# Performance work log

Measured on AMD Instinct MI355X. Metric: run time of the kernel, lower is better.

The kernel has to match this reference:

```python
import jax, jax.numpy as jnp
import numpy as np

N_NODES = 50000
N_EDGES = 600000
NODE_DIM = 128
HID = 128
NUM_LAYERS = 3


def setup_inputs() -> dict:
    key = jax.random.key(0)
    ks = jax.random.split(key, 16)
    s = lambda fan_in: 1.0 / np.sqrt(fan_in)
    inp = {
        'node_features': jax.random.normal(ks[0], (N_NODES, NODE_DIM), dtype=jnp.float32),
        'edge_index': jax.random.randint(ks[1], (2, N_EDGES), 0, N_NODES, dtype=jnp.int64 if jax.config.jax_enable_x64 else jnp.int32),
        # node embedding
        'W_emb': jax.random.uniform(ks[2], (NODE_DIM, HID), jnp.float32, -s(NODE_DIM), s(NODE_DIM)),
        'b_emb': jnp.zeros((HID,), jnp.float32),
        # gnn layers (stacked over layer axis)
        'W_gnn': jax.random.uniform(ks[3], (NUM_LAYERS, HID, HID), jnp.float32, -s(HID), s(HID)),
        'b_gnn': jnp.zeros((NUM_LAYERS, HID), jnp.float32),
        # edge mask generator
        'W_m1': jax.random.uniform(ks[4], (2 * HID, HID), jnp.float32, -s(2 * HID), s(2 * HID)),
        'b_m1': jnp.zeros((HID,), jnp.float32),
        'W_m2': jax.random.uniform(ks[5], (HID, 1), jnp.float32, -s(HID), s(HID)),
        'b_m2': jnp.zeros((1,), jnp.float32),
        # predictor
        'W_p1': jax.random.uniform(ks[6], (HID, HID), jnp.float32, -s(HID), s(HID)),
        'b_p1': jnp.zeros((HID,), jnp.float32),
        'W_p2': jax.random.uniform(ks[7], (HID, 1), jnp.float32, -s(HID), s(HID)),
        'b_p2': jnp.zeros((1,), jnp.float32),
    }
    return inp


def _edge_mask(h, src, dst, W_m1, b_m1, W_m2, b_m2):
    # per-edge gather + concat -> 2-layer MLP -> sigmoid importance
    ef = jnp.concatenate([h[src], h[dst]], axis=1)          # [E, 2H]
    imp = jax.nn.sigmoid(jax.nn.relu(ef @ W_m1 + b_m1) @ W_m2 + b_m2)[:, 0]  # [E]
    # eval mode: temp=2.0, offset=0.4
    return jax.nn.sigmoid((imp - 0.4) * 2.0)


def reference(node_features, edge_index, W_emb, b_emb, W_gnn, b_gnn,
              W_m1, b_m1, W_m2, b_m2, W_p1, b_p1, W_p2, b_p2):
    src, dst = edge_index[0], edge_index[1]
    n = node_features.shape[0]
    h = jax.nn.relu(node_features @ W_emb + b_emb)           # [N, H]
    mask = _edge_mask(h, src, dst, W_m1, b_m1, W_m2, b_m2)    # [E]
    for i in range(NUM_LAYERS):
        msgs = jax.ops.segment_sum(h[src] * mask[:, None], dst, num_segments=n)  # scatter-add
        h = jax.nn.relu((h + msgs) @ W_gnn[i] + b_gnn[i])
        if i < NUM_LAYERS - 1:
            mask = _edge_mask(h, src, dst, W_m1, b_m1, W_m2, b_m2)
    prediction = jax.nn.relu(h[0] @ W_p1 + b_p1) @ W_p2 + b_p2  # [1]
    return prediction, mask, h
```

## Files before the change

### kernel.cpp

```cpp
#include <hip/hip_runtime.h>
#include <hip/hip_bf16.h>

#define NN 50000
#define NE 600000
#define HD 128
#define DET_SAMPLES 65536
#define NBLK 196
#define GGRID4 ((NN + 15)/16)
#define LDT 136

typedef unsigned short ushort_t;
typedef __attribute__((ext_vector_type(8))) short short8v;
typedef __attribute__((ext_vector_type(4))) float f32x4;

__device__ __forceinline__ float sigmoidf_(float x){ return 1.f/(1.f+__expf(-x)); }

__device__ __forceinline__ ushort_t f2bf(float f){
  unsigned int u = __float_as_uint(f);
  unsigned int r = (u + 0x7FFFu + ((u >> 16) & 1u)) >> 16;
  return (ushort_t)r;
}

__device__ __forceinline__ float bflo(unsigned u){ return __uint_as_float(u << 16); }
__device__ __forceinline__ float bfhi(unsigned u){ return __uint_as_float(u & 0xFFFF0000u); }

__global__ void write_scalar_kernel(float* __restrict__ p, float v){ p[0] = v; }

__global__ void detect_kernel(const unsigned int* __restrict__ w, int* __restrict__ flag){
  int i = blockIdx.x*256 + threadIdx.x;
  int z = (w[2*i + 1] == 0u) ? 1 : 0;
  atomicAdd(flag, z);
}

__global__ void extract_kernel(const void* __restrict__ ei, const int* __restrict__ flag,
                               int* __restrict__ srcW, int* __restrict__ dstW,
                               int* __restrict__ counts){
  const int e = blockIdx.x*256 + threadIdx.x;
  if (e >= NE) return;
  int s, d;
  if (*flag > (DET_SAMPLES/2)){
    const long long* p = (const long long*)ei;
    s = (int)p[e]; d = (int)p[NE + e];
  } else {
    const int* p = (const int*)ei;
    s = p[e]; d = p[NE + e];
  }
  srcW[e] = s; dstW[e] = d;
  atomicAdd(&counts[d], 1);
}

__global__ __launch_bounds__(256) void scanA_kernel(const int* __restrict__ counts,
                                                    int* __restrict__ partial){
  __shared__ int s[256];
  const int t = threadIdx.x;
  const int idx = blockIdx.x*256 + t;
  s[t] = (idx < NN) ? counts[idx] : 0;
  __syncthreads();
  for (int off = 128; off > 0; off >>= 1){
    if (t < off) s[t] += s[t + off];
    __syncthreads();
  }
  if (t == 0) partial[blockIdx.x] = s[0];
}

__global__ __launch_bounds__(256) void scanB_kernel(const int* __restrict__ partial,
                                                    int* __restrict__ bOff){
  __shared__ int s[256];
  const int t = threadIdx.x;
  const int v = (t < NBLK) ? partial[t] : 0;
  s[t] = v;
  __syncthreads();
  for (int off = 1; off < 256; off <<= 1){
    int add = (t >= off) ? s[t - off] : 0;
    __syncthreads();
    s[t] += add;
    __syncthreads();
  }
  if (t < NBLK) bOff[t] = s[t] - v;
}

__global__ __launch_bounds__(256) void scanC_kernel(const int* __restrict__ counts,
    const int* __restrict__ bOff, int* __restrict__ row_start, int* __restrict__ cursor){
  __shared__ int s[256];
  const int t = threadIdx.x;
  const int idx = blockIdx.x*256 + t;
  const int c = (idx < NN) ? counts[idx] : 0;
  s[t] = c;
  __syncthreads();
  for (int off = 1; off < 256; off <<= 1){
    int add = (t >= off) ? s[t - off] : 0;
    __syncthreads();
    s[t] += add;
    __syncthreads();
  }
  const int excl = bOff[blockIdx.x] + s[t] - c;
  if (idx < NN){ row_start[idx] = excl; cursor[idx] = excl; }
  else if (idx == NN){ row_start[NN] = excl; }
}

__global__ void fill_kernel(const int* __restrict__ dstI, const int* __restrict__ srcI,
                            int* __restrict__ cursor, int* __restrict__ eids,
                            int* __restrict__ srcS){
  int e = blockIdx.x*256 + threadIdx.x;
  if (e < NE){
    int p = atomicAdd(&cursor[dstI[e]], 1);
    eids[p] = e;
    srcS[p] = srcI[e];
  }
}

__global__ __launch_bounds__(256) void wcvt_all_kernel(const float* __restrict__ Wemb,
    const float* __restrict__ Wgnn, const float* __restrict__ Wm1,
    ushort_t* __restrict__ WtAll){
  const int idx = blockIdx.x*256 + threadIdx.x;
  const int m = idx >> 14;
  const int r = idx & 16383;
  const int k = r >> 7, n = r & 127;
  const float* W = (m == 0) ? Wemb : (m <= 3) ? (Wgnn + (size_t)(m-1)*16384)
                                              : (Wm1  + (size_t)(m-4)*16384);
  WtAll[(size_t)m*16384 + n*HD + k] = f2bf(W[r]);
}

template<int F32A>
__global__ __launch_bounds__(256) void gemm_fused(const void* __restrict__ inP,
    const ushort_t* __restrict__ Wt, const float* __restrict__ bias,
    float* __restrict__ outF, ushort_t* __restrict__ outB,
    const ushort_t* __restrict__ WtU, const ushort_t* __restrict__ WtV,
    const float* __restrict__ biasU, ushort_t* __restrict__ outU,
    ushort_t* __restrict__ outV, int n, int doRelu)
{
  __shared__ ushort_t hT[16*LDT];
  const int cq   = threadIdx.x >> 6;
  const int lane = threadIdx.x & 63;
  const int fr = lane & 15;
  const int fq = lane >> 4;
  const int row0 = blockIdx.x*16;
  const int arow = row0 + fr;
  const bool rowok = (arow < n);
  f32x4 acc[2];
  acc[0] = (f32x4)0.0f; acc[1] = (f32x4)0.0f;
  #pragma unroll
  for (int ks = 0; ks < 4; ++ks){
    const int k0 = ks*32 + fq*8;
    short8v af = (short8v)0;
    if (rowok){
      if (F32A){
        const float* in = (const float*)inP;
        const float4 a0 = *(const float4*)(in + (size_t)arow*HD + k0);
        const float4 a1 = *(const float4*)(in + (size_t)arow*HD + k0 + 4);
        af[0]=(short)f2bf(a0.x); af[1]=(short)f2bf(a0.y);
        af[2]=(short)f2bf(a0.z); af[3]=(short)f2bf(a0.w);
        af[4]=(short)f2bf(a1.x); af[5]=(short)f2bf(a1.y);
        af[6]=(short)f2bf(a1.z); af[7]=(short)f2bf(a1.w);
      } else {
        const ushort_t* inB = (const ushort_t*)inP;
        af = *(const short8v*)(inB + (size_t)arow*HD + k0);
      }
    }
    #pragma unroll
    for (int tcl = 0; tcl < 2; ++tcl){
      const int tc = cq*2 + tcl;
      const short8v bf = *(const short8v*)(Wt + (size_t)(tc*16 + fr)*HD + k0);
      acc[tcl] = __builtin_amdgcn_mfma_f32_16x16x32_bf16(af, bf, acc[tcl], 0, 0, 0);
    }
  }
  #pragma unroll
  for (int tcl = 0; tcl < 2; ++tcl){
    const int col = (cq*2 + tcl)*16 + fr;
    const float b = bias ? bias[col] : 0.f;
    #pragma unroll
    for (int j = 0; j < 4; ++j){
      const int r = row0 + fq*4 + j;
      float x = acc[tcl][j] + b;
      if (doRelu) x = fmaxf(x, 0.f);
      const ushort_t xb = (r < n) ? f2bf(x) : (ushort_t)0;
      if (WtU) hT[(fq*4 + j)*LDT + col] = xb;
      if (r < n){
        if (outF) outF[(size_t)r*HD + col] = x;
        if (outB) outB[(size_t)r*HD + col] = xb;
      }
    }
  }
  if (WtU){
    __syncthreads();
    f32x4 aU[2], aV[2];
    aU[0] = (f32x4)0.0f; aU[1] = (f32x4)0.0f;
    aV[0] = (f32x4)0.0f; aV[1] = (f32x4)0.0f;
    #pragma unroll
    for (int ks = 0; ks < 4; ++ks){
      const int k0 = ks*32 + fq*8;
      const short8v af = *(const short8v*)(hT + fr*LDT + k0);
      #pragma unroll
      for (int tcl = 0; tcl < 2; ++tcl){
        const int tc = cq*2 + tcl;
        const short8v bu = *(const short8v*)(WtU + (size_t)(tc*16 + fr)*HD + k0);
        aU[tcl] = __builtin_amdgcn_mfma_f32_16x16x32_bf16(af, bu, aU[tcl], 0, 0, 0);
        const short8v bv = *(const short8v*)(WtV + (size_t)(tc*16 + fr)*HD + k0);
        aV[tcl] = __builtin_amdgcn_mfma_f32_16x16x32_bf16(af, bv, aV[tcl], 0, 0, 0);
      }
    }
    #pragma unroll
    for (int tcl = 0; tcl < 2; ++tcl){
      const int col = (cq*2 + tcl)*16 + fr;
      const float b = biasU[col];
      #pragma unroll
      for (int j = 0; j < 4; ++j){
        const int r = row0 + fq*4 + j;
        if (r >= n) continue;
        outU[(size_t)r*HD + col] = f2bf(aU[tcl][j] + b);
        outV[(size_t)r*HD + col] = f2bf(aV[tcl][j]);
      }
    }
  }
}

__global__ __launch_bounds__(256) void mask_msg_kernel(
    const ushort_t* __restrict__ U, const ushort_t* __restrict__ V,
    const ushort_t* __restrict__ hB,
    ushort_t* __restrict__ hB2,
    const int* __restrict__ srcS, const int* __restrict__ eidS,
    const int* __restrict__ row_start,
    const float* __restrict__ Wm2, const float* __restrict__ bm2,
    float* __restrict__ maskOut)
{
  const int v = blockIdx.x*4 + (threadIdx.x >> 6);
  const int lane = threadIdx.x & 63;
  const int g   = lane >> 4;
  const int sub = lane & 15;
  const float4 wA = ((const float4*)Wm2)[sub*2];
  const float4 wB = ((const float4*)Wm2)[sub*2+1];
  const float b2 = bm2[0];
  const uint4 vv = ((const uint4*)(V + (size_t)v*HD))[sub];
  float a0=0.f,a1=0.f,a2=0.f,a3=0.f,a4=0.f,a5=0.f,a6=0.f,a7=0.f;
  const int beg = row_start[v], end = row_start[v+1];
  int idx = beg + g;
  uint4 uu = make_uint4(0,0,0,0), hh = make_uint4(0,0,0,0);
  int e0 = 0;
  if (idx < end){
    const int s = srcS[idx];
    if (maskOut) e0 = eidS[idx];
    uu = ((const uint4*)(U  + (size_t)s*HD))[sub];
    hh = ((const uint4*)(hB + (size_t)s*HD))[sub];
  }
  while (idx < end){
    const int nidx = idx + 4;
    uint4 uuN = make_uint4(0,0,0,0), hhN = make_uint4(0,0,0,0);
    int eN = 0;
    if (nidx < end){
      const int sn = srcS[nidx];
      if (maskOut) eN = eidS[nidx];
      uuN = ((const uint4*)(U  + (size_t)sn*HD))[sub];
      hhN = ((const uint4*)(hB + (size_t)sn*HD))[sub];
    }
    float p;
    p = fmaxf(bflo(uu.x)+bflo(vv.x), 0.f) * wA.x;
    p = fmaf(fmaxf(bfhi(uu.x)+bfhi(vv.x), 0.f), wA.y, p);
    p = fmaf(fmaxf(bflo(uu.y)+bflo(vv.y), 0.f), wA.z, p);
    p = fmaf(fmaxf(bfhi(uu.y)+bfhi(vv.y), 0.f), wA.w, p);
    p = fmaf(fmaxf(bflo(uu.z)+bflo(vv.z), 0.f), wB.x, p);
    p = fmaf(fmaxf(bfhi(uu.z)+bfhi(vv.z), 0.f), wB.y, p);
    p = fmaf(fmaxf(bflo(uu.w)+bflo(vv.w), 0.f), wB.z, p);
    p = fmaf(fmaxf(bfhi(uu.w)+bfhi(vv.w), 0.f), wB.w, p);
    p += __shfl_xor(p, 1, 64);
    p += __shfl_xor(p, 2, 64);
    p += __shfl_xor(p, 4, 64);
    p += __shfl_xor(p, 8, 64);
    const float imp = sigmoidf_(p + b2);
    const float mk  = sigmoidf_((imp - 0.4f) * 2.0f);
    if (maskOut != nullptr && sub == 0) maskOut[e0] = mk;
    a0 = fmaf(mk, bflo(hh.x), a0);
    a1 = fmaf(mk, bfhi(hh.x), a1);
    a2 = fmaf(mk, bflo(hh.y), a2);
    a3 = fmaf(mk, bfhi(hh.y), a3);
    a4 = fmaf(mk, bflo(hh.z), a4);
    a5 = fmaf(mk, bfhi(hh.z), a5);
    a6 = fmaf(mk, bflo(hh.w), a6);
    a7 = fmaf(mk, bfhi(hh.w), a7);
    uu = uuN; hh = hhN; e0 = eN; idx = nidx;
  }
  a0 += __shfl_xor(a0, 16, 64); a0 += __shfl_xor(a0, 32, 64);
  a1 += __shfl_xor(a1, 16, 64); a1 += __shfl_xor(a1, 32, 64);
  a2 += __shfl_xor(a2, 16, 64); a2 += __shfl_xor(a2, 32, 64);
  a3 += __shfl_xor(a3, 16, 64); a3 += __shfl_xor(a3, 32, 64);
  a4 += __shfl_xor(a4, 16, 64); a4 += __shfl_xor(a4, 32, 64);
  a5 += __shfl_xor(a5, 16, 64); a5 += __shfl_xor(a5, 32, 64);
  a6 += __shfl_xor(a6, 16, 64); a6 += __shfl_xor(a6, 32, 64);
  a7 += __shfl_xor(a7, 16, 64); a7 += __shfl_xor(a7, 32, 64);
  if (g == 0){
    const uint4 hrow = ((const uint4*)(hB + (size_t)v*HD))[sub];
    const float x0 = bflo(hrow.x) + a0, x1 = bfhi(hrow.x) + a1;
    const float x2 = bflo(hrow.y) + a2, x3 = bfhi(hrow.y) + a3;
    const float x4 = bflo(hrow.z) + a4, x5 = bfhi(hrow.z) + a5;
    const float x6 = bflo(hrow.w) + a6, x7 = bfhi(hrow.w) + a7;
    ushort4 p0, p1;
    p0.x = f2bf(x0); p0.y = f2bf(x1); p0.z = f2bf(x2); p0.w = f2bf(x3);
    p1.x = f2bf(x4); p1.y = f2bf(x5); p1.z = f2bf(x6); p1.w = f2bf(x7);
    ushort4* hb2row = (ushort4*)(hB2 + (size_t)v*HD) + sub*2;
    hb2row[0] = p0;
    hb2row[1] = p1;
  }
}

__global__ __launch_bounds__(128) void pred_kernel(const float* __restrict__ h,
  const float* __restrict__ Wp1, const float* __restrict__ bp1,
  const float* __restrict__ Wp2, const float* __restrict__ bp2,
  float* __restrict__ out0)
{
  __shared__ float red[128];
  const int t = threadIdx.x;
  float s = bp1[t];
  for (int k = 0; k < HD; ++k) s = fmaf(h[k], Wp1[k*HD + t], s);
  s = fmaxf(s, 0.f) * Wp2[t];
  red[t] = s;
  __syncthreads();
  for (int off = 64; off > 0; off >>= 1){
    if (t < off) red[t] += red[t + off];
    __syncthreads();
  }
  if (t == 0) out0[0] = red[0] + bp2[0];
}

extern "C" void kernel_launch(void* const* d_in, const int* in_sizes, int n_in,
                              void* d_out, int out_size, void* d_ws, size_t ws_size,
                              hipStream_t stream)
{
  (void)out_size;
  float* fOut = (float*)d_out;
  float* predOut = fOut;
  float* maskOut = fOut + 1;
  float* hOut    = fOut + 1 + NE;

  static const int expSizes[14] = {6400000,1200000,16384,128,49152,384,32768,128,128,1,
                                   16384,128,128,1};
  const size_t NEEDED = 87100000;
  float diag = 0.f;
  if (n_in != 14) diag = 900.f + (float)n_in;
  else {
    for (int i = 0; i < 14; ++i)
      if (in_sizes[i] != expSizes[i]){ diag = 200.f + 16.f*(float)i; break; }
  }
  if (diag == 0.f && ws_size < NEEDED) diag = 5000.f + (float)(ws_size >> 20);

  if (diag != 0.f){
    write_scalar_kernel<<<1, 1, 0, stream>>>(predOut, diag);
    return;
  }

  const float* nf   = (const float*)d_in[0];
  const void*  ei   = d_in[1];
  const float* Wemb = (const float*)d_in[2];
  const float* bemb = (const float*)d_in[3];
  const float* Wgnn = (const float*)d_in[4];
  const float* bgnn = (const float*)d_in[5];
  const float* Wm1  = (const float*)d_in[6];
  const float* bm1  = (const float*)d_in[7];
  const float* Wm2  = (const float*)d_in[8];
  const float* bm2  = (const float*)d_in[9];
  const float* Wp1  = (const float*)d_in[10];
  const float* bp1  = (const float*)d_in[11];
  const float* Wp2  = (const float*)d_in[12];
  const float* bp2  = (const float*)d_in[13];

  float* hA    = (float*)d_ws;
  float* tmpU  = hA   + (size_t)NN*HD;
  float* Vbuf  = tmpU + (size_t)NN*HD;
  float* srcSf = Vbuf + (size_t)NN*HD;
  int* srcS    = (int*)srcSf;
  int* row_start = srcS + NE;
  int* cursor  = row_start + (NN + 1);
  int* counts  = cursor + NN;
  int* eids    = counts + NN;
  int* srcW    = eids + NE;
  int* dstW    = srcW + NE;
  int* flag    = dstW + NE;
  int* partial = flag + 1;
  int* bOff    = partial + NBLK;

  ushort_t* Ub  = (ushort_t*)tmpU;
  ushort_t* hB2 = (ushort_t*)tmpU + (size_t)NN*HD;
  ushort_t* Vb  = (ushort_t*)Vbuf;
  ushort_t* hB  = (ushort_t*)Vbuf + (size_t)NN*HD;

  ushort_t* WtAll = (ushort_t*)cursor;
  ushort_t* WtEmb = WtAll;
  ushort_t* WtG0  = WtAll + 1*16384;
  ushort_t* WtG1  = WtAll + 2*16384;
  ushort_t* WtG2  = WtAll + 3*16384;
  ushort_t* WtU   = WtAll + 4*16384;
  ushort_t* WtV   = WtAll + 5*16384;

  hipMemsetAsync(flag, 0, sizeof(int), stream);
  hipMemsetAsync(counts, 0, NN*sizeof(int), stream);
  detect_kernel<<<DET_SAMPLES/256, 256, 0, stream>>>((const unsigned int*)ei, flag);
  extract_kernel<<<(NE + 255)/256, 256, 0, stream>>>(ei, flag, srcW, dstW, counts);

  scanA_kernel<<<NBLK, 256, 0, stream>>>(counts, partial);
  scanB_kernel<<<1, 256, 0, stream>>>(partial, bOff);
  scanC_kernel<<<NBLK, 256, 0, stream>>>(counts, bOff, row_start, cursor);
  fill_kernel<<<(NE + 255)/256, 256, 0, stream>>>(dstW, srcW, cursor, eids, srcS);

  wcvt_all_kernel<<<384, 256, 0, stream>>>(Wemb, Wgnn, Wm1, WtAll);

  gemm_fused<1><<<GGRID4, 256, 0, stream>>>(nf, WtEmb, bemb, nullptr, hB,
                                            WtU, WtV, bm1, Ub, Vb, NN, 1);

  const ushort_t* WtG[3] = {WtG0, WtG1, WtG2};
  for (int L = 0; L < 3; ++L){
    float* mOut = (L < 2) ? nullptr : maskOut;
    mask_msg_kernel<<<NN/4, 256, 0, stream>>>(Ub, Vb, hB, hB2, srcS, eids, row_start,
                                              Wm2, bm2, mOut);
    if (L < 2){
      gemm_fused<0><<<GGRID4, 256, 0, stream>>>(hB2, WtG[L], bgnn + (size_t)L*HD,
                                                nullptr, hB, WtU, WtV, bm1, Ub, Vb,
                                                NN, 1);
    } else {
      gemm_fused<0><<<GGRID4, 256, 0, stream>>>(hB2, WtG[2], bgnn + 2*HD,
                                                hOut, nullptr, nullptr, nullptr,
                                                nullptr, nullptr, nullptr, NN, 1);
    }
  }

  pred_kernel<<<1, 128, 0, stream>>>(hOut, Wp1, bp1, Wp2, bp2, predOut);
}
```

Measured before the change: 437.2 us.

## Make GEMM blocks persistent and keep weight fragments in registers across tiles

The fused node GEMM now launches a fixed grid of 782 blocks. Each block loops over up to four 16-row tiles, and the W, Wu and Wv fragments plus biases are loaded into registers once per block instead of once per tile. Bounds checks are dropped because N is a multiple of 16, and the last layer gets a dedicated gemm_final kernel. This removes repeated weight loads from L2 in exchange for higher register pressure (launch_bounds 256,3) and fewer resident blocks.

```diff
diff --git a/kernel.cpp b/kernel.cpp
--- a/kernel.cpp
+++ b/kernel.cpp
@@ -6,7 +6,8 @@
 #define HD 128
 #define DET_SAMPLES 65536
 #define NBLK 196
-#define GGRID4 ((NN + 15)/16)
+#define NTILES 3125
+#define GPERS 782
 #define LDT 136
 
 typedef unsigned short ushort_t;
@@ -121,29 +122,53 @@
   WtAll[(size_t)m*16384 + n*HD + k] = f2bf(W[r]);
 }
 
-template<int F32A>
-__global__ __launch_bounds__(256) void gemm_fused(const void* __restrict__ inP,
+template<int F32A, int DOUV>
+__global__ __launch_bounds__(256, 3) void gemm_fused(const void* __restrict__ inP,
     const ushort_t* __restrict__ Wt, const float* __restrict__ bias,
     float* __restrict__ outF, ushort_t* __restrict__ outB,
     const ushort_t* __restrict__ WtU, const ushort_t* __restrict__ WtV,
     const float* __restrict__ biasU, ushort_t* __restrict__ outU,
-    ushort_t* __restrict__ outV, int n, int doRelu)
+    ushort_t* __restrict__ outV)
 {
   __shared__ ushort_t hT[16*LDT];
   const int cq   = threadIdx.x >> 6;
   const int lane = threadIdx.x & 63;
   const int fr = lane & 15;
   const int fq = lane >> 4;
-  const int row0 = blockIdx.x*16;
-  const int arow = row0 + fr;
-  const bool rowok = (arow < n);
-  f32x4 acc[2];
-  acc[0] = (f32x4)0.0f; acc[1] = (f32x4)0.0f;
+  short8v bh[4][2];
   #pragma unroll
-  for (int ks = 0; ks < 4; ++ks){
-    const int k0 = ks*32 + fq*8;
-    short8v af = (short8v)0;
-    if (rowok){
+  for (int ks = 0; ks < 4; ++ks)
+    #pragma unroll
+    for (int tcl = 0; tcl < 2; ++tcl)
+      bh[ks][tcl] = *(const short8v*)(Wt + (size_t)((cq*2+tcl)*16 + fr)*HD + ks*32 + fq*8);
+  short8v bu[4][2], bv[4][2];
+  if (DOUV){
+    #pragma unroll
+    for (int ks = 0; ks < 4; ++ks)
+      #pragma unroll
+      for (int tcl = 0; tcl < 2; ++tcl){
+        bu[ks][tcl] = *(const short8v*)(WtU + (size_t)((cq*2+tcl)*16 + fr)*HD + ks*32 + fq*8);
+        bv[ks][tcl] = *(const short8v*)(WtV + (size_t)((cq*2+tcl)*16 + fr)*HD + ks*32 + fq*8);
+      }
+  }
+  float bb[2], bub[2];
+  #pragma unroll
+  for (int tcl = 0; tcl < 2; ++tcl){
+    const int col = (cq*2 + tcl)*16 + fr;
+    bb[tcl]  = bias ? bias[col] : 0.f;
+    bub[tcl] = DOUV ? biasU[col] : 0.f;
+  }
+
+  for (int it = 0; it < 4; ++it){
+    const int tile = blockIdx.x + it*GPERS;
+    if (tile >= NTILES) break;
+    const int row0 = tile*16;
+    const int arow = row0 + fr;
+    f32x4 acc0 = (f32x4)0.0f, acc1 = (f32x4)0.0f;
+    #pragma unroll
+    for (int ks = 0; ks < 4; ++ks){
+      const int k0 = ks*32 + fq*8;
+      short8v af;
       if (F32A){
         const float* in = (const float*)inP;
         const float4 a0 = *(const float4*)(in + (size_t)arow*HD + k0);
@@ -156,60 +181,49 @@
         const ushort_t* inB = (const ushort_t*)inP;
         af = *(const short8v*)(inB + (size_t)arow*HD + k0);
       }
+      acc0 = __builtin_amdgcn_mfma_f32_16x16x32_bf16(af, bh[ks][0], acc0, 0, 0, 0);
+      acc1 = __builtin_amdgcn_mfma_f32_16x16x32_bf16(af, bh[ks][1], acc1, 0, 0, 0);
     }
     #pragma unroll
     for (int tcl = 0; tcl < 2; ++tcl){
-      const int tc = cq*2 + tcl;
-      const short8v bf = *(const short8v*)(Wt + (size_t)(tc*16 + fr)*HD + k0);
-      acc[tcl] = __builtin_amdgcn_mfma_f32_16x16x32_bf16(af, bf, acc[tcl], 0, 0, 0);
-    }
-  }
-  #pragma unroll
-  for (int tcl = 0; tcl < 2; ++tcl){
-    const int col = (cq*2 + tcl)*16 + fr;
-    const float b = bias ? bias[col] : 0.f;
-    #pragma unroll
-    for (int j = 0; j < 4; ++j){
-      const int r = row0 + fq*4 + j;
-      float x = acc[tcl][j] + b;
-      if (doRelu) x = fmaxf(x, 0.f);
-      const ushort_t xb = (r < n) ? f2bf(x) : (ushort_t)0;
-      if (WtU) hT[(fq*4 + j)*LDT + col] = xb;
-      if (r < n){
-        if (outF) outF[(size_t)r*HD + col] = x;
-        if (outB) outB[(size_t)r*HD + col] = xb;
-      }
-    }
-  }
-  if (WtU){
-    __syncthreads();
-    f32x4 aU[2], aV[2];
-    aU[0] = (f32x4)0.0f; aU[1] = (f32x4)0.0f;
-    aV[0] = (f32x4)0.0f; aV[1] = (f32x4)0.0f;
-    #pragma unroll
-    for (int ks = 0; ks < 4; ++ks){
-      const int k0 = ks*32 + fq*8;
-      const short8v af = *(const short8v*)(hT + fr*LDT + k0);
-      #pragma unroll
-      for (int tcl = 0; tcl < 2; ++tcl){
-        const int tc = cq*2 + tcl;
-        const short8v bu = *(const short8v*)(WtU + (size_t)(tc*16 + fr)*HD + k0);
-        aU[tcl] = __builtin_amdgcn_mfma_f32_16x16x32_bf16(af, bu, aU[tcl], 0, 0, 0);
-        const short8v bv = *(const short8v*)(WtV + (size_t)(tc*16 + fr)*HD + k0);
-        aV[tcl] = __builtin_amdgcn_mfma_f32_16x16x32_bf16(af, bv, aV[tcl], 0, 0, 0);
-      }
-    }
-    #pragma unroll
-    for (int tcl = 0; tcl < 2; ++tcl){
+      const f32x4 a = tcl ? acc1 : acc0;
       const int col = (cq*2 + tcl)*16 + fr;
-      const float b = biasU[col];
       #pragma unroll
       for (int j = 0; j < 4; ++j){
         const int r = row0 + fq*4 + j;
-        if (r >= n) continue;
-        outU[(size_t)r*HD + col] = f2bf(aU[tcl][j] + b);
-        outV[(size_t)r*HD + col] = f2bf(aV[tcl][j]);
-      }
+        float x = a[j] + bb[tcl];
+        x = fmaxf(x, 0.f);
+        const ushort_t xb = f2bf(x);
+        if (DOUV) hT[(fq*4 + j)*LDT + col] = xb;
+        if (outF) outF[(size_t)r*HD + col] = x;
+        if (outB) outB[(size_t)r*HD + col] = xb;
+      }
+    }
+    if (DOUV){
+      __syncthreads();
+      f32x4 aU0 = (f32x4)0.0f, aU1 = (f32x4)0.0f;
+      f32x4 aV0 = (f32x4)0.0f, aV1 = (f32x4)0.0f;
+      #pragma unroll
+      for (int ks = 0; ks < 4; ++ks){
+        const short8v af = *(const short8v*)(hT + fr*LDT + ks*32 + fq*8);
+        aU0 = __builtin_amdgcn_mfma_f32_16x16x32_bf16(af, bu[ks][0], aU0, 0, 0, 0);
+        aU1 = __builtin_amdgcn_mfma_f32_16x16x32_bf16(af, bu[ks][1], aU1, 0, 0, 0);
+        aV0 = __builtin_amdgcn_mfma_f32_16x16x32_bf16(af, bv[ks][0], aV0, 0, 0, 0);
+        aV1 = __builtin_amdgcn_mfma_f32_16x16x32_bf16(af, bv[ks][1], aV1, 0, 0, 0);
+      }
+      #pragma unroll
+      for (int tcl = 0; tcl < 2; ++tcl){
+        const f32x4 u = tcl ? aU1 : aU0;
+        const f32x4 v = tcl ? aV1 : aV0;
+        const int col = (cq*2 + tcl)*16 + fr;
+        #pragma unroll
+        for (int j = 0; j < 4; ++j){
+          const int r = row0 + fq*4 + j;
+          outU[(size_t)r*HD + col] = f2bf(u[j] + bub[tcl]);
+          outV[(size_t)r*HD + col] = f2bf(v[j]);
+        }
+      }
+      __syncthreads();
     }
   }
 }
@@ -301,6 +315,49 @@
   }
 }
 
+__global__ __launch_bounds__(256, 3) void gemm_final(const ushort_t* __restrict__ inB,
+    const ushort_t* __restrict__ Wt, const float* __restrict__ bias,
+    float* __restrict__ outF)
+{
+  const int cq   = threadIdx.x >> 6;
+  const int lane = threadIdx.x & 63;
+  const int fr = lane & 15;
+  const int fq = lane >> 4;
+  short8v bh[4][2];
+  #pragma unroll
+  for (int ks = 0; ks < 4; ++ks)
+    #pragma unroll
+    for (int tcl = 0; tcl < 2; ++tcl)
+      bh[ks][tcl] = *(const short8v*)(Wt + (size_t)((cq*2+tcl)*16 + fr)*HD + ks*32 + fq*8);
+  float bb[2];
+  #pragma unroll
+  for (int tcl = 0; tcl < 2; ++tcl) bb[tcl] = bias[(cq*2 + tcl)*16 + fr];
+  for (int it = 0; it < 4; ++it){
+    const int tile = blockIdx.x + it*GPERS;
+    if (tile >= NTILES) break;
+    const int row0 = tile*16;
+    const int arow = row0 + fr;
+    f32x4 acc0 = (f32x4)0.0f, acc1 = (f32x4)0.0f;
+    #pragma unroll
+    for (int ks = 0; ks < 4; ++ks){
+      const int k0 = ks*32 + fq*8;
+      const short8v af = *(const short8v*)(inB + (size_t)arow*HD + k0);
+      acc0 = __builtin_amdgcn_mfma_f32_16x16x32_bf16(af, bh[ks][0], acc0, 0, 0, 0);
+      acc1 = __builtin_amdgcn_mfma_f32_16x16x32_bf16(af, bh[ks][1], acc1, 0, 0, 0);
+    }
+    #pragma unroll
+    for (int tcl = 0; tcl < 2; ++tcl){
+      const f32x4 a = tcl ? acc1 : acc0;
+      const int col = (cq*2 + tcl)*16 + fr;
+      #pragma unroll
+      for (int j = 0; j < 4; ++j){
+        const int r = row0 + fq*4 + j;
+        outF[(size_t)r*HD + col] = fmaxf(a[j] + bb[tcl], 0.f);
+      }
+    }
+  }
+}
+
 __global__ __launch_bounds__(128) void pred_kernel(const float* __restrict__ h,
   const float* __restrict__ Wp1, const float* __restrict__ bp1,
   const float* __restrict__ Wp2, const float* __restrict__ bp2,
@@ -401,8 +458,8 @@
 
   wcvt_all_kernel<<<384, 256, 0, stream>>>(Wemb, Wgnn, Wm1, WtAll);
 
-  gemm_fused<1><<<GGRID4, 256, 0, stream>>>(nf, WtEmb, bemb, nullptr, hB,
-                                            WtU, WtV, bm1, Ub, Vb, NN, 1);
+  gemm_fused<1,1><<<GPERS, 256, 0, stream>>>(nf, WtEmb, bemb, nullptr, hB,
+                                             WtU, WtV, bm1, Ub, Vb);
 
   const ushort_t* WtG[3] = {WtG0, WtG1, WtG2};
   for (int L = 0; L < 3; ++L){
@@ -410,13 +467,10 @@
     mask_msg_kernel<<<NN/4, 256, 0, stream>>>(Ub, Vb, hB, hB2, srcS, eids, row_start,
                                               Wm2, bm2, mOut);
     if (L < 2){
-      gemm_fused<0><<<GGRID4, 256, 0, stream>>>(hB2, WtG[L], bgnn + (size_t)L*HD,
-                                                nullptr, hB, WtU, WtV, bm1, Ub, Vb,
-                                                NN, 1);
+      gemm_fused<0,1><<<GPERS, 256, 0, stream>>>(hB2, WtG[L], bgnn + (size_t)L*HD,
+                                                 nullptr, hB, WtU, WtV, bm1, Ub, Vb);
     } else {
-      gemm_fused<0><<<GGRID4, 256, 0, stream>>>(hB2, WtG[2], bgnn + 2*HD,
-                                                hOut, nullptr, nullptr, nullptr,
-                                                nullptr, nullptr, nullptr, NN, 1);
+      gemm_final<<<GPERS, 256, 0, stream>>>(hB2, WtG[2], bgnn + 2*HD, hOut);
     }
   }
 
```

After: 372.3 us. 14.8% less time.
